# Performance work log

Hardware: AMD Instinct MI355X
Metric: run time of the kernel (lower is better)

Reference implementation:

```python
import jax, jax.numpy as jnp
import numpy as np

# dims
Z, P, N, H = 16, 4, 466, 86          # z_dim, p_dim, n_dim, gmean(466,16)
B_SZ, T = 2048, 32                   # batch, number of eval times
INNER = 16                           # fixed trial-step budget per eval interval
ATOL, RTOL = 1e-20, 1e-5
H2B, H3B = 64, 2048                  # B-net hiddens: int(sqrt(16**3)), 16**3//2

# Dormand-Prince 5(4) tableau
A21 = 1/5
A31, A32 = 3/40, 9/40
A41, A42, A43 = 44/45, -56/15, 32/9
A51, A52, A53, A54 = 19372/6561, -25360/2187, 64448/6561, -212/729
A61, A62, A63, A64, A65 = 9017/3168, -355/33, 46732/5247, 49/176, -5103/18656
B1, B3, B4, B5, B6 = 35/384, 500/1113, 125/192, -2187/6784, 11/84
E1, E3, E4, E5, E6, E7 = 71/57600, -71/16695, 71/1920, -17253/339200, 22/525, -1/40


def _leaky(x):
    return jnp.where(x >= 0, x, 0.2 * x)


def setup_inputs() -> dict:
    key = jax.random.key(0)
    ks = jax.random.split(key, 26)
    w = lambda k, shape: (jax.random.normal(k, shape) * 0.05).astype(jnp.float32)
    inp = {}
    inp['n_0'] = jax.random.normal(ks[0], (B_SZ, N), dtype=jnp.float32)
    inp['p'] = jax.random.uniform(ks[1], (P,), dtype=jnp.float32)
    inp['tstep'] = jnp.arange(T, dtype=jnp.float32) / (T - 1)
    # autoencoder
    inp['We1'], inp['be1'] = w(ks[2], (N, H)), w(ks[3], (H,))
    inp['We2'], inp['be2'] = w(ks[4], (H, Z)), w(ks[5], (Z,))
    inp['Wd1'], inp['bd1'] = w(ks[6], (Z, H)), w(ks[7], (H,))
    inp['Wd2'], inp['bd2'] = w(ks[8], (H, N)), w(ks[9], (N,))
    # A net: P -> Z -> Z*Z//2 -> Z*Z
    inp['Wa1'], inp['ba1'] = w(ks[10], (P, Z)), w(ks[11], (Z,))
    inp['Wa2'], inp['ba2'] = w(ks[12], (Z, Z*Z//2)), w(ks[13], (Z*Z//2,))
    inp['Wa3'], inp['ba3'] = w(ks[14], (Z*Z//2, Z*Z)), w(ks[15], (Z*Z,))
    # B net: P -> Z -> 64 -> 2048 -> Z**3
    inp['Wb1'], inp['bb1'] = w(ks[16], (P, Z)), w(ks[17], (Z,))
    inp['Wb2'], inp['bb2'] = w(ks[18], (Z, H2B)), w(ks[19], (H2B,))
    inp['Wb3'], inp['bb3'] = w(ks[20], (H2B, H3B)), w(ks[21], (H3B,))
    inp['Wb4'], inp['bb4'] = w(ks[22], (H3B, Z**3)), w(ks[23], (Z**3,))
    return inp


def _solve(z0, tstep, Amat, Bten):
    # adaptive Dopri5 with integral (I) step-size controller; fixed trial budget per interval
    def f(z):  # g(z,p): A z + B z z
        return z @ Amat.T + jnp.einsum('ijk,bj,bk->bi', Bten, z, z)

    def step(y, dt):
        k1 = f(y)
        k2 = f(y + dt * (A21 * k1))
        k3 = f(y + dt * (A31 * k1 + A32 * k2))
        k4 = f(y + dt * (A41 * k1 + A42 * k2 + A43 * k3))
        k5 = f(y + dt * (A51 * k1 + A52 * k2 + A53 * k3 + A54 * k4))
        k6 = f(y + dt * (A61 * k1 + A62 * k2 + A63 * k3 + A64 * k4 + A65 * k5))
        y5 = y + dt * (B1 * k1 + B3 * k3 + B4 * k4 + B5 * k5 + B6 * k6)
        k7 = f(y5)
        err = dt * (E1 * k1 + E3 * k3 + E4 * k4 + E5 * k5 + E6 * k6 + E7 * k7)
        return y5, err

    def interval(carry, tpair):
        y, dt = carry
        t0, t1 = tpair[0], tpair[1]

        def inner(c, _):
            t, y, dt = c
            done = t >= t1 - 1e-10
            dtc = jnp.where(done, 0.0, jnp.minimum(dt, t1 - t))  # clip to interval end
            ynew, err = step(y, dtc)
            tol = ATOL + RTOL * jnp.maximum(jnp.abs(y), jnp.abs(ynew))
            en = jnp.sqrt(jnp.mean((err / tol) ** 2))
            accept = (en <= 1.0) & (~done)
            t = jnp.where(accept, t + dtc, t)
            y = jnp.where(accept, ynew, y)
            factor = jnp.clip(0.9 * jnp.maximum(en, 1e-12) ** -0.2, 0.2, 10.0)
            dt = jnp.where(done, dt, dt * factor)
            return (t, y, dt), None

        (tf, yf, dtf), _ = jax.lax.scan(inner, (t0, y, dt), None, length=INNER)
        return (yf, dtf), yf

    dt0 = (tstep[1] - tstep[0]) * 0.3
    tpairs = jnp.stack([tstep[:-1], tstep[1:]], axis=1)  # [T-1, 2]
    (_, _), ys = jax.lax.scan(interval, (z0, dt0), tpairs)
    return jnp.concatenate([z0[None], ys], axis=0)  # [T, b, Z]


def reference(n_0, p, tstep, We1, be1, We2, be2, Wd1, bd1, Wd2, bd2,
              Wa1, ba1, Wa2, ba2, Wa3, ba3,
              Wb1, bb1, Wb2, bb2, Wb3, bb3, Wb4, bb4):
    # encoder
    z0 = _leaky(n_0 @ We1 + be1) @ We2 + be2  # [b, Z]
    # A(p), B(p) depend only on p -> computed once per solve
    ha = _leaky(p @ Wa1 + ba1)
    ha = _leaky(ha @ Wa2 + ba2)
    Amat = _leaky(ha @ Wa3 + ba3).reshape(Z, Z)
    hb = _leaky(p @ Wb1 + bb1)
    hb = _leaky(hb @ Wb2 + bb2)
    hb = _leaky(hb @ Wb3 + bb3)
    Bten = _leaky(hb @ Wb4 + bb4).reshape(Z, Z, Z)
    zs = _solve(z0, tstep, Amat, Bten)  # [T, b, Z]
    # decoder
    return _leaky(zs @ Wd1 + bd1) @ Wd2 + bd2  # [T, b, N]
```

## Files before the change

kernel.cpp:

```cpp
#include <hip/hip_runtime.h>
#include <cmath>

#define DEV __device__ __forceinline__

static DEV float leakyf(float x){ return x >= 0.0f ? x : 0.2f*x; }

typedef float v2f __attribute__((ext_vector_type(2)));

constexpr float cA21 = (float)(1.0/5.0);
constexpr float cA31 = (float)(3.0/40.0),  cA32 = (float)(9.0/40.0);
constexpr float cA41 = (float)(44.0/45.0), cA42 = (float)(-56.0/15.0), cA43 = (float)(32.0/9.0);
constexpr float cA51 = (float)(19372.0/6561.0), cA52 = (float)(-25360.0/2187.0);
constexpr float cA53 = (float)(64448.0/6561.0), cA54 = (float)(-212.0/729.0);
constexpr float cA61 = (float)(9017.0/3168.0),  cA62 = (float)(-355.0/33.0);
constexpr float cA63 = (float)(46732.0/5247.0), cA64 = (float)(49.0/176.0);
constexpr float cA65 = (float)(-5103.0/18656.0);
constexpr float cB1 = (float)(35.0/384.0),  cB3 = (float)(500.0/1113.0), cB4 = (float)(125.0/192.0);
constexpr float cB5 = (float)(-2187.0/6784.0), cB6 = (float)(11.0/84.0);
constexpr float cE1 = (float)(71.0/57600.0), cE3 = (float)(-71.0/16695.0), cE4 = (float)(71.0/1920.0);
constexpr float cE5 = (float)(-17253.0/339200.0), cE6 = (float)(22.0/525.0), cE7 = (float)(-1.0/40.0);

#define WS_AMAT   0
#define WS_HB3    256
#define WS_BTEN   2304
#define WS_ZS     6400
#define WS_SLOTSF (6400 + 1048576)
#define WS_SB2    (WS_SLOTSF + 253952)

template<int CTRL>
static DEV float dpp_add(float v){
    int x = __builtin_amdgcn_update_dpp(0, __float_as_int(v), CTRL, 0xf, 0xf, true);
    return v + __int_as_float(x);
}
static DEV float wave_sum_frozen(float w){
    w = dpp_add<0xB1>(w);
    w = dpp_add<0x4E>(w);
    w = dpp_add<0x141>(w);
    w = dpp_add<0x140>(w);
    int b = __float_as_int(w);
    float q0 = __int_as_float(__builtin_amdgcn_readlane(b, 0));
    float q1 = __int_as_float(__builtin_amdgcn_readlane(b, 16));
    float q2 = __int_as_float(__builtin_amdgcn_readlane(b, 32));
    float q3 = __int_as_float(__builtin_amdgcn_readlane(b, 48));
    return (q0 + q1) + (q2 + q3);
}

__global__ void __launch_bounds__(256) k_smallnets(
    const float* __restrict__ p,
    const float* __restrict__ Wa1, const float* __restrict__ ba1,
    const float* __restrict__ Wa2, const float* __restrict__ ba2,
    const float* __restrict__ Wa3, const float* __restrict__ ba3,
    const float* __restrict__ Wb1, const float* __restrict__ bb1,
    const float* __restrict__ Wb2, const float* __restrict__ bb2,
    float* __restrict__ wsf)
{
    __shared__ float sp[4], sa1[16], sa2[128], sb1[16];
    int tid = threadIdx.x;
    if (tid < 4) sp[tid] = p[tid];
    __syncthreads();
    if (tid < 16) {
        float a = ba1[tid];
        for (int j = 0; j < 4; ++j) a = fmaf(sp[j], Wa1[j*16+tid], a);
        sa1[tid] = leakyf(a);
        float c = bb1[tid];
        for (int j = 0; j < 4; ++j) c = fmaf(sp[j], Wb1[j*16+tid], c);
        sb1[tid] = leakyf(c);
    }
    __syncthreads();
    if (tid < 128) {
        float a = ba2[tid];
        for (int j = 0; j < 16; ++j) a = fmaf(sa1[j], Wa2[j*128+tid], a);
        sa2[tid] = leakyf(a);
    }
    if (tid < 64) {
        float c = bb2[tid];
        for (int j = 0; j < 16; ++j) c = fmaf(sb1[j], Wb2[j*64+tid], c);
        wsf[WS_SB2 + tid] = leakyf(c);
    }
    __syncthreads();
    {
        float a = ba3[tid];
        for (int j = 0; j < 128; ++j) a = fmaf(sa2[j], Wa3[j*256+tid], a);
        wsf[WS_AMAT + tid] = leakyf(a);
    }
}

__global__ void __launch_bounds__(256) k_hb3(
    const float* __restrict__ Wb3, const float* __restrict__ bb3, float* __restrict__ wsf)
{
    __shared__ float sb2[64];
    int tid = threadIdx.x;
    if (tid < 64) sb2[tid] = wsf[WS_SB2 + tid];
    __syncthreads();
    int o = blockIdx.x * 256 + tid;
    float c = bb3[o];
    for (int j = 0; j < 64; ++j) c = fmaf(sb2[j], Wb3[(size_t)j*2048 + o], c);
    wsf[WS_HB3 + o] = leakyf(c);
}

__global__ void __launch_bounds__(256) k_bten(
    const float* __restrict__ Wb4, const float* __restrict__ bb4, float* __restrict__ wsf)
{
    __shared__ float red[256];
    const float* hb3 = wsf + WS_HB3;
    float* Bten = wsf + WS_BTEN;
    int tid = threadIdx.x;
    int ol = tid & 15, part = tid >> 4;
    int o = blockIdx.x * 16 + ol;
    float a = 0.0f;
    for (int q = 0; q < 128; ++q) {
        int hh = part*128 + q;
        a = fmaf(hb3[hh], Wb4[(size_t)hh*4096 + o], a);
    }
    red[part*16 + ol] = a;
    __syncthreads();
    for (int s = 8; s >= 1; s >>= 1) {
        if (part < s) red[part*16+ol] += red[(part+s)*16+ol];
        __syncthreads();
    }
    if (tid < 16) {
        float v = red[tid] + bb4[blockIdx.x*16 + tid];
        Bten[blockIdx.x*16 + tid] = leakyf(v);
    }
}

__global__ void __launch_bounds__(256) k_solver(
    const float* __restrict__ tstep,
    const float* __restrict__ n0,
    const float* __restrict__ We1, const float* __restrict__ be1,
    const float* __restrict__ We2, const float* __restrict__ be2,
    float* __restrict__ wsf)
{
    __shared__ float hE[8][88];
    __shared__ float zE[8][16];
    __shared__ float zL[8][16];
    __shared__ float redA[2][4], redB[2][4];
    float* Amat = wsf + WS_AMAT;
    float* Bten = wsf + WS_BTEN;
    float* zs   = wsf + WS_ZS;
    unsigned long long* slots = (unsigned long long*)(wsf + WS_SLOTSF);

    const int tid = threadIdx.x, blk = blockIdx.x;
    const int e = tid >> 5, g = tid & 31;
    const int i = g >> 1, h = g & 1, h8 = h * 8;
    const int b = blk * 8 + e;

    {
        int r = tid >> 5, c = tid & 31;
        int row = blk * 8 + r;
        const float* nrow = n0 + (size_t)row * 466;
        int c2 = (c + 64 < 86) ? (c + 64) : 85;
        float a0 = 0.f, a1 = 0.f, a2 = 0.f;
        for (int n = 0; n < 466; ++n) {
            float nv = nrow[n];
            a0 = fmaf(nv, We1[n*86 + c], a0);
            a1 = fmaf(nv, We1[n*86 + c + 32], a1);
            a2 = fmaf(nv, We1[n*86 + c2], a2);
        }
        hE[r][c]      = leakyf(a0 + be1[c]);
        hE[r][c + 32] = leakyf(a1 + be1[c + 32]);
        if (c < 22) hE[r][c + 64] = leakyf(a2 + be1[c + 64]);
        __syncthreads();
        if (tid < 128) {
            int r2 = tid >> 4, ii = tid & 15;
            float a = be2[ii];
            #pragma unroll
            for (int hh = 0; hh < 86; ++hh) a = fmaf(hE[r2][hh], We2[hh*16 + ii], a);
            zE[r2][ii] = a;
            zs[((size_t)(blk*8 + r2)) * 16 + ii] = a;
        }
        __syncthreads();
    }

    v2f Bl2[64], aR2[8];
    #pragma unroll
    for (int p = 0; p < 8; ++p) {
        int jA = (h8 + 2*p)     & 15;
        int jB = (h8 + 2*p + 1) & 15;
        v2f ap; ap.x = (h == 0) ? Amat[i*16 + 2*p] : 0.0f;
        ap.y = (h == 0) ? Amat[i*16 + 2*p + 1] : 0.0f;
        aR2[p] = ap;
        const float4* bpA = (const float4*)(Bten + i*256 + jA*16 + h8);
        const float4* bpB = (const float4*)(Bten + i*256 + jB*16 + h8);
        float4 a0 = bpA[0], a1 = bpA[1], b0 = bpB[0], b1 = bpB[1];
        v2f q;
        q.x=a0.x; q.y=b0.x; Bl2[p*8+0]=q;  q.x=a0.y; q.y=b0.y; Bl2[p*8+1]=q;
        q.x=a0.z; q.y=b0.z; Bl2[p*8+2]=q;  q.x=a0.w; q.y=b0.w; Bl2[p*8+3]=q;
        q.x=a1.x; q.y=b1.x; Bl2[p*8+4]=q;  q.x=a1.y; q.y=b1.y; Bl2[p*8+5]=q;
        q.x=a1.z; q.y=b1.z; Bl2[p*8+6]=q;  q.x=a1.w; q.y=b1.w; Bl2[p*8+7]=q;
    }

    float y = zE[e][i];

    auto feval = [&](float zi) -> float {
        zL[e][i] = zi;
        const float4* zp = (const float4*)(&zL[e][0]);
        int q0 = h8 >> 2;
        float4 r0 = zp[q0], r1 = zp[(q0+1)&3], r2 = zp[(q0+2)&3], r3 = zp[(q0+3)&3];
        float zz[16] = { r0.x,r0.y,r0.z,r0.w, r1.x,r1.y,r1.z,r1.w,
                         r2.x,r2.y,r2.z,r2.w, r3.x,r3.y,r3.z,r3.w };
        v2f zb[8];
        #pragma unroll
        for (int kk = 0; kk < 8; ++kk) { v2f t; t.x = zz[kk]; t.y = zz[kk]; zb[kk] = t; }
        v2f t2[8];
        #pragma unroll
        for (int p = 0; p < 8; ++p) t2[p] = aR2[p];
        #pragma unroll
        for (int p = 0; p < 8; ++p) {
            #pragma unroll
            for (int kk = 0; kk < 8; ++kk)
                asm("v_pk_fma_f32 %0, %1, %2, %0" : "+v"(t2[p]) : "v"(Bl2[p*8+kk]), "v"(zb[kk]));
        }
        float acc = 0.0f;
        #pragma unroll
        for (int p = 0; p < 8; ++p) {
            acc = fmaf(zz[2*p],     t2[p].x, acc);
            acc = fmaf(zz[2*p + 1], t2[p].y, acc);
        }
        acc = dpp_add<0xB1>(acc);
        return acc;
    };

    float dt = (tstep[1] - tstep[0]) * 0.3f;
    float k1 = feval(y), k2, k3, k4, k5, k6, k7;
    int stepIdx = 0;

    for (int iv = 0; iv < 31; ++iv) {
        float t  = tstep[iv];
        float t1 = tstep[iv + 1];
        for (int it = 0; it < 16; ++it) {
            if (t >= t1 - 1e-10f) break;
            float dtc = fminf(dt, t1 - t);

            float z2 = fmaf(dtc, cA21*k1, y);                                         k2 = feval(z2);
            float z3 = fmaf(dtc, fmaf(cA32,k2, cA31*k1), y);                          k3 = feval(z3);
            float z4 = fmaf(dtc, fmaf(cA43,k3, fmaf(cA42,k2, cA41*k1)), y);           k4 = feval(z4);
            float z5 = fmaf(dtc, fmaf(cA54,k4, fmaf(cA53,k3, fmaf(cA52,k2, cA51*k1))), y);
            k5 = feval(z5);
            float z6 = fmaf(dtc, fmaf(cA65,k5, fmaf(cA64,k4, fmaf(cA63,k3, fmaf(cA62,k2, cA61*k1)))), y);
            k6 = feval(z6);
            float y5 = fmaf(dtc, fmaf(cB6,k6, fmaf(cB5,k5, fmaf(cB4,k4, fmaf(cB3,k3, cB1*k1)))), y);
            k7 = feval(y5);
            float err = dtc * fmaf(cE7,k7, fmaf(cE6,k6, fmaf(cE5,k5, fmaf(cE4,k4, fmaf(cE3,k3, cE1*k1)))));

            float ay = fabsf(y), a5 = fabsf(y5);
            float mx = (ay > a5) ? ay : a5;
            float tol = fmaf(1e-5f, mx, 1e-20f);
            float r = err / tol;
            float r2 = r * r;

            const int par = stepIdx & 1;

            float w = wave_sum_frozen(r2);
            if ((tid & 63) == 0) redA[par][tid >> 6] = w;
            __syncthreads();
            float bsum = ((redA[par][0] + redA[par][1]) + redA[par][2]) + redA[par][3];

            unsigned long long* rowp = slots + (size_t)stepIdx * 256;
            if (tid == 0) {
                unsigned long long pv = (1ull << 32) | (unsigned long long)__float_as_uint(bsum);
                __hip_atomic_store(&rowp[blk], pv, __ATOMIC_RELAXED, __HIP_MEMORY_SCOPE_AGENT);
            }
            unsigned long long v = __hip_atomic_load(&rowp[tid], __ATOMIC_RELAXED, __HIP_MEMORY_SCOPE_AGENT);
            if ((unsigned)(v >> 32) != 1u) {
                for (;;) {
                    unsigned long long va = __hip_atomic_load(&rowp[tid], __ATOMIC_RELAXED, __HIP_MEMORY_SCOPE_AGENT);
                    unsigned long long vb = __hip_atomic_load(&rowp[tid], __ATOMIC_RELAXED, __HIP_MEMORY_SCOPE_AGENT);
                    if ((unsigned)(va >> 32) == 1u) { v = va; break; }
                    if ((unsigned)(vb >> 32) == 1u) { v = vb; break; }
                }
            }
            float ps = wave_sum_frozen(__uint_as_float((unsigned)v));
            if ((tid & 63) == 0) redB[par][tid >> 6] = ps;
            __syncthreads();
            float gsum = ((redB[par][0] + redB[par][1]) + redB[par][2]) + redB[par][3];
            ++stepIdx;

            float en = sqrtf(gsum * (1.0f / 65536.0f));

            if (!(en == en)) {
                if (h == 0) {
                    for (int s = iv + 1; s < 32; ++s)
                        zs[((size_t)s * 2048 + b) * 16 + i] = y;
                }
                return;
            }
            if (en <= 1.0f) { t = t + dtc; y = y5; k1 = k7; }
            float fac = 0.9f * powf(fmaxf(en, 1e-12f), -0.2f);
            fac = fminf(fmaxf(fac, 0.2f), 10.0f);
            dt = dt * fac;
        }
        if (h == 0) zs[((size_t)(iv + 1) * 2048 + b) * 16 + i] = y;
    }
}

__global__ void __launch_bounds__(256) k_decoder(
    const float* __restrict__ zs,
    const float* __restrict__ Wd1, const float* __restrict__ bd1,
    const float* __restrict__ Wd2, const float* __restrict__ bd2,
    float* __restrict__ out)
{
    __shared__ __align__(16) float hT[86][16];
    int tid = threadIdx.x;
    size_t rowbase = (size_t)blockIdx.x * 16;

    for (int v = tid; v < 86*16; v += 256) {
        int hh = v >> 4, r = v & 15;
        const float4* z4 = (const float4*)(zs + (rowbase + r) * 16);
        float4 za = z4[0], zb = z4[1], zc = z4[2], zd = z4[3];
        float a = bd1[hh];
        a = fmaf(za.x, Wd1[ 0*86 + hh], a);  a = fmaf(za.y, Wd1[ 1*86 + hh], a);
        a = fmaf(za.z, Wd1[ 2*86 + hh], a);  a = fmaf(za.w, Wd1[ 3*86 + hh], a);
        a = fmaf(zb.x, Wd1[ 4*86 + hh], a);  a = fmaf(zb.y, Wd1[ 5*86 + hh], a);
        a = fmaf(zb.z, Wd1[ 6*86 + hh], a);  a = fmaf(zb.w, Wd1[ 7*86 + hh], a);
        a = fmaf(zc.x, Wd1[ 8*86 + hh], a);  a = fmaf(zc.y, Wd1[ 9*86 + hh], a);
        a = fmaf(zc.z, Wd1[10*86 + hh], a);  a = fmaf(zc.w, Wd1[11*86 + hh], a);
        a = fmaf(zd.x, Wd1[12*86 + hh], a);  a = fmaf(zd.y, Wd1[13*86 + hh], a);
        a = fmaf(zd.z, Wd1[14*86 + hh], a);  a = fmaf(zd.w, Wd1[15*86 + hh], a);
        hT[hh][r] = leakyf(a);
    }
    __syncthreads();

    for (int c = tid; c < 466; c += 256) {
        float acc[16];
        #pragma unroll
        for (int r = 0; r < 16; ++r) acc[r] = bd2[c];
        for (int hh = 0; hh < 86; ++hh) {
            float w = Wd2[hh*466 + c];
            const float4* hp = (const float4*)(&hT[hh][0]);
            float4 h0 = hp[0], h1 = hp[1], h2 = hp[2], h3 = hp[3];
            acc[ 0] = fmaf(h0.x, w, acc[ 0]);  acc[ 1] = fmaf(h0.y, w, acc[ 1]);
            acc[ 2] = fmaf(h0.z, w, acc[ 2]);  acc[ 3] = fmaf(h0.w, w, acc[ 3]);
            acc[ 4] = fmaf(h1.x, w, acc[ 4]);  acc[ 5] = fmaf(h1.y, w, acc[ 5]);
            acc[ 6] = fmaf(h1.z, w, acc[ 6]);  acc[ 7] = fmaf(h1.w, w, acc[ 7]);
            acc[ 8] = fmaf(h2.x, w, acc[ 8]);  acc[ 9] = fmaf(h2.y, w, acc[ 9]);
            acc[10] = fmaf(h2.z, w, acc[10]);  acc[11] = fmaf(h2.w, w, acc[11]);
            acc[12] = fmaf(h3.x, w, acc[12]);  acc[13] = fmaf(h3.y, w, acc[13]);
            acc[14] = fmaf(h3.z, w, acc[14]);  acc[15] = fmaf(h3.w, w, acc[15]);
        }
        #pragma unroll
        for (int r = 0; r < 16; ++r) out[(rowbase + r) * 466 + c] = acc[r];
    }
}

extern "C" void kernel_launch(void* const* d_in, const int* in_sizes, int n_in,
                              void* d_out, int out_size, void* d_ws, size_t ws_size,
                              hipStream_t stream)
{
    const float* n0   = (const float*)d_in[0];
    const float* p    = (const float*)d_in[1];
    const float* tstep= (const float*)d_in[2];
    const float* We1  = (const float*)d_in[3];  const float* be1 = (const float*)d_in[4];
    const float* We2  = (const float*)d_in[5];  const float* be2 = (const float*)d_in[6];
    const float* Wd1  = (const float*)d_in[7];  const float* bd1 = (const float*)d_in[8];
    const float* Wd2  = (const float*)d_in[9];  const float* bd2 = (const float*)d_in[10];
    const float* Wa1  = (const float*)d_in[11]; const float* ba1 = (const float*)d_in[12];
    const float* Wa2  = (const float*)d_in[13]; const float* ba2 = (const float*)d_in[14];
    const float* Wa3  = (const float*)d_in[15]; const float* ba3 = (const float*)d_in[16];
    const float* Wb1  = (const float*)d_in[17]; const float* bb1 = (const float*)d_in[18];
    const float* Wb2  = (const float*)d_in[19]; const float* bb2 = (const float*)d_in[20];
    const float* Wb3  = (const float*)d_in[21]; const float* bb3 = (const float*)d_in[22];
    const float* Wb4  = (const float*)d_in[23]; const float* bb4 = (const float*)d_in[24];
    float* out = (float*)d_out;
    float* wsf = (float*)d_ws;

    hipLaunchKernelGGL(k_smallnets, dim3(1), dim3(256), 0, stream,
                       p, Wa1, ba1, Wa2, ba2, Wa3, ba3, Wb1, bb1, Wb2, bb2, wsf);
    hipLaunchKernelGGL(k_hb3, dim3(8), dim3(256), 0, stream, Wb3, bb3, wsf);
    hipLaunchKernelGGL(k_bten, dim3(256), dim3(256), 0, stream, Wb4, bb4, wsf);

    hipLaunchKernelGGL(k_solver, dim3(256), dim3(256), 0, stream,
                       tstep, n0, We1, be1, We2, be2, wsf);

    hipLaunchKernelGGL(k_decoder, dim3(4096), dim3(256), 0, stream,
                       wsf + WS_ZS, Wd1, bd1, Wd2, bd2, out);
}
```

Baseline: 1.254 ms.

## Fuse small parameter nets into bten and solver kernels, removing two launches

```diff
diff --git a/kernel.cpp b/kernel.cpp
--- a/kernel.cpp
+++ b/kernel.cpp
@@ -20,12 +20,9 @@
 constexpr float cE1 = (float)(71.0/57600.0), cE3 = (float)(-71.0/16695.0), cE4 = (float)(71.0/1920.0);
 constexpr float cE5 = (float)(-17253.0/339200.0), cE6 = (float)(22.0/525.0), cE7 = (float)(-1.0/40.0);
 
-#define WS_AMAT   0
-#define WS_HB3    256
 #define WS_BTEN   2304
 #define WS_ZS     6400
 #define WS_SLOTSF (6400 + 1048576)
-#define WS_SB2    (WS_SLOTSF + 253952)
 
 template<int CTRL>
 static DEV float dpp_add(float v){
@@ -45,66 +42,42 @@
     return (q0 + q1) + (q2 + q3);
 }
 
-__global__ void __launch_bounds__(256) k_smallnets(
+__global__ void __launch_bounds__(256) k_bten(
     const float* __restrict__ p,
-    const float* __restrict__ Wa1, const float* __restrict__ ba1,
-    const float* __restrict__ Wa2, const float* __restrict__ ba2,
-    const float* __restrict__ Wa3, const float* __restrict__ ba3,
     const float* __restrict__ Wb1, const float* __restrict__ bb1,
     const float* __restrict__ Wb2, const float* __restrict__ bb2,
+    const float* __restrict__ Wb3, const float* __restrict__ bb3,
+    const float* __restrict__ Wb4, const float* __restrict__ bb4,
     float* __restrict__ wsf)
 {
-    __shared__ float sp[4], sa1[16], sa2[128], sb1[16];
+    __shared__ float sp[4], sb1[16], sb2[64];
+    __shared__ float hb3[2048];
+    __shared__ float red[256];
+    float* Bten = wsf + WS_BTEN;
     int tid = threadIdx.x;
+
     if (tid < 4) sp[tid] = p[tid];
     __syncthreads();
     if (tid < 16) {
-        float a = ba1[tid];
-        for (int j = 0; j < 4; ++j) a = fmaf(sp[j], Wa1[j*16+tid], a);
-        sa1[tid] = leakyf(a);
         float c = bb1[tid];
         for (int j = 0; j < 4; ++j) c = fmaf(sp[j], Wb1[j*16+tid], c);
         sb1[tid] = leakyf(c);
     }
     __syncthreads();
-    if (tid < 128) {
-        float a = ba2[tid];
-        for (int j = 0; j < 16; ++j) a = fmaf(sa1[j], Wa2[j*128+tid], a);
-        sa2[tid] = leakyf(a);
-    }
     if (tid < 64) {
         float c = bb2[tid];
         for (int j = 0; j < 16; ++j) c = fmaf(sb1[j], Wb2[j*64+tid], c);
-        wsf[WS_SB2 + tid] = leakyf(c);
-    }
-    __syncthreads();
-    {
-        float a = ba3[tid];
-        for (int j = 0; j < 128; ++j) a = fmaf(sa2[j], Wa3[j*256+tid], a);
-        wsf[WS_AMAT + tid] = leakyf(a);
-    }
-}
-
-__global__ void __launch_bounds__(256) k_hb3(
-    const float* __restrict__ Wb3, const float* __restrict__ bb3, float* __restrict__ wsf)
-{
-    __shared__ float sb2[64];
-    int tid = threadIdx.x;
-    if (tid < 64) sb2[tid] = wsf[WS_SB2 + tid];
-    __syncthreads();
-    int o = blockIdx.x * 256 + tid;
-    float c = bb3[o];
-    for (int j = 0; j < 64; ++j) c = fmaf(sb2[j], Wb3[(size_t)j*2048 + o], c);
-    wsf[WS_HB3 + o] = leakyf(c);
-}
-
-__global__ void __launch_bounds__(256) k_bten(
-    const float* __restrict__ Wb4, const float* __restrict__ bb4, float* __restrict__ wsf)
-{
-    __shared__ float red[256];
-    const float* hb3 = wsf + WS_HB3;
-    float* Bten = wsf + WS_BTEN;
-    int tid = threadIdx.x;
+        sb2[tid] = leakyf(c);
+    }
+    __syncthreads();
+    for (int q = 0; q < 8; ++q) {
+        int o = q*256 + tid;
+        float c = bb3[o];
+        for (int j = 0; j < 64; ++j) c = fmaf(sb2[j], Wb3[(size_t)j*2048 + o], c);
+        hb3[o] = leakyf(c);
+    }
+    __syncthreads();
+
     int ol = tid & 15, part = tid >> 4;
     int o = blockIdx.x * 16 + ol;
     float a = 0.0f;
@@ -129,13 +102,17 @@
     const float* __restrict__ n0,
     const float* __restrict__ We1, const float* __restrict__ be1,
     const float* __restrict__ We2, const float* __restrict__ be2,
+    const float* __restrict__ p,
+    const float* __restrict__ Wa1, const float* __restrict__ ba1,
+    const float* __restrict__ Wa2, const float* __restrict__ ba2,
+    const float* __restrict__ Wa3, const float* __restrict__ ba3,
     float* __restrict__ wsf)
 {
     __shared__ float hE[8][88];
     __shared__ float zE[8][16];
     __shared__ float zL[8][16];
+    __shared__ float sp[4], sa1[16], sa2[128], sAmat[256];
     __shared__ float redA[2][4], redB[2][4];
-    float* Amat = wsf + WS_AMAT;
     float* Bten = wsf + WS_BTEN;
     float* zs   = wsf + WS_ZS;
     unsigned long long* slots = (unsigned long long*)(wsf + WS_SLOTSF);
@@ -144,6 +121,29 @@
     const int e = tid >> 5, g = tid & 31;
     const int i = g >> 1, h = g & 1, h8 = h * 8;
     const int b = blk * 8 + e;
+
+    {
+        if (tid < 4) sp[tid] = p[tid];
+        __syncthreads();
+        if (tid < 16) {
+            float a = ba1[tid];
+            for (int j = 0; j < 4; ++j) a = fmaf(sp[j], Wa1[j*16+tid], a);
+            sa1[tid] = leakyf(a);
+        }
+        __syncthreads();
+        if (tid < 128) {
+            float a = ba2[tid];
+            for (int j = 0; j < 16; ++j) a = fmaf(sa1[j], Wa2[j*128+tid], a);
+            sa2[tid] = leakyf(a);
+        }
+        __syncthreads();
+        {
+            float a = ba3[tid];
+            for (int j = 0; j < 128; ++j) a = fmaf(sa2[j], Wa3[j*256+tid], a);
+            sAmat[tid] = leakyf(a);
+        }
+        __syncthreads();
+    }
 
     {
         int r = tid >> 5, c = tid & 31;
@@ -174,20 +174,20 @@
 
     v2f Bl2[64], aR2[8];
     #pragma unroll
-    for (int p = 0; p < 8; ++p) {
-        int jA = (h8 + 2*p)     & 15;
-        int jB = (h8 + 2*p + 1) & 15;
-        v2f ap; ap.x = (h == 0) ? Amat[i*16 + 2*p] : 0.0f;
-        ap.y = (h == 0) ? Amat[i*16 + 2*p + 1] : 0.0f;
-        aR2[p] = ap;
+    for (int p2 = 0; p2 < 8; ++p2) {
+        int jA = (h8 + 2*p2)     & 15;
+        int jB = (h8 + 2*p2 + 1) & 15;
+        v2f ap; ap.x = (h == 0) ? sAmat[i*16 + 2*p2] : 0.0f;
+        ap.y = (h == 0) ? sAmat[i*16 + 2*p2 + 1] : 0.0f;
+        aR2[p2] = ap;
         const float4* bpA = (const float4*)(Bten + i*256 + jA*16 + h8);
         const float4* bpB = (const float4*)(Bten + i*256 + jB*16 + h8);
         float4 a0 = bpA[0], a1 = bpA[1], b0 = bpB[0], b1 = bpB[1];
         v2f q;
-        q.x=a0.x; q.y=b0.x; Bl2[p*8+0]=q;  q.x=a0.y; q.y=b0.y; Bl2[p*8+1]=q;
-        q.x=a0.z; q.y=b0.z; Bl2[p*8+2]=q;  q.x=a0.w; q.y=b0.w; Bl2[p*8+3]=q;
-        q.x=a1.x; q.y=b1.x; Bl2[p*8+4]=q;  q.x=a1.y; q.y=b1.y; Bl2[p*8+5]=q;
-        q.x=a1.z; q.y=b1.z; Bl2[p*8+6]=q;  q.x=a1.w; q.y=b1.w; Bl2[p*8+7]=q;
+        q.x=a0.x; q.y=b0.x; Bl2[p2*8+0]=q;  q.x=a0.y; q.y=b0.y; Bl2[p2*8+1]=q;
+        q.x=a0.z; q.y=b0.z; Bl2[p2*8+2]=q;  q.x=a0.w; q.y=b0.w; Bl2[p2*8+3]=q;
+        q.x=a1.x; q.y=b1.x; Bl2[p2*8+4]=q;  q.x=a1.y; q.y=b1.y; Bl2[p2*8+5]=q;
+        q.x=a1.z; q.y=b1.z; Bl2[p2*8+6]=q;  q.x=a1.w; q.y=b1.w; Bl2[p2*8+7]=q;
     }
 
     float y = zE[e][i];
@@ -204,18 +204,18 @@
         for (int kk = 0; kk < 8; ++kk) { v2f t; t.x = zz[kk]; t.y = zz[kk]; zb[kk] = t; }
         v2f t2[8];
         #pragma unroll
-        for (int p = 0; p < 8; ++p) t2[p] = aR2[p];
-        #pragma unroll
-        for (int p = 0; p < 8; ++p) {
+        for (int p2 = 0; p2 < 8; ++p2) t2[p2] = aR2[p2];
+        #pragma unroll
+        for (int p2 = 0; p2 < 8; ++p2) {
             #pragma unroll
             for (int kk = 0; kk < 8; ++kk)
-                asm("v_pk_fma_f32 %0, %1, %2, %0" : "+v"(t2[p]) : "v"(Bl2[p*8+kk]), "v"(zb[kk]));
+                asm("v_pk_fma_f32 %0, %1, %2, %0" : "+v"(t2[p2]) : "v"(Bl2[p2*8+kk]), "v"(zb[kk]));
         }
         float acc = 0.0f;
         #pragma unroll
-        for (int p = 0; p < 8; ++p) {
-            acc = fmaf(zz[2*p],     t2[p].x, acc);
-            acc = fmaf(zz[2*p + 1], t2[p].y, acc);
+        for (int p2 = 0; p2 < 8; ++p2) {
+            acc = fmaf(zz[2*p2],     t2[p2].x, acc);
+            acc = fmaf(zz[2*p2 + 1], t2[p2].y, acc);
         }
         acc = dpp_add<0xB1>(acc);
         return acc;
@@ -364,13 +364,12 @@
     float* out = (float*)d_out;
     float* wsf = (float*)d_ws;
 
-    hipLaunchKernelGGL(k_smallnets, dim3(1), dim3(256), 0, stream,
-                       p, Wa1, ba1, Wa2, ba2, Wa3, ba3, Wb1, bb1, Wb2, bb2, wsf);
-    hipLaunchKernelGGL(k_hb3, dim3(8), dim3(256), 0, stream, Wb3, bb3, wsf);
-    hipLaunchKernelGGL(k_bten, dim3(256), dim3(256), 0, stream, Wb4, bb4, wsf);
+    hipLaunchKernelGGL(k_bten, dim3(256), dim3(256), 0, stream,
+                       p, Wb1, bb1, Wb2, bb2, Wb3, bb3, Wb4, bb4, wsf);
 
     hipLaunchKernelGGL(k_solver, dim3(256), dim3(256), 0, stream,
-                       tstep, n0, We1, be1, We2, be2, wsf);
+                       tstep, n0, We1, be1, We2, be2,
+                       p, Wa1, ba1, Wa2, ba2, Wa3, ba3, wsf);
 
     hipLaunchKernelGGL(k_decoder, dim3(4096), dim3(256), 0, stream,
                        wsf + WS_ZS, Wd1, bd1, Wd2, bd2, out);
```

Measured after the change: 1.344 ms. +7.2%, slower.
